# Kernel tuning notes

Hardware: AMD Instinct MI355X
Metric: run time of the kernel (lower is better)

The kernel has to match this reference:

```python
import jax, jax.numpy as jnp
import numpy as np

N, F = 8000, 256
NEG_SLOPE = 0.2


def setup_inputs() -> dict:
    key = jax.random.key(0)
    k1, k2, k3, k4, k5, k6, k7 = jax.random.split(key, 7)
    node_embeddings = jax.random.normal(k1, (N, F), dtype=jnp.float32)
    adj_matrix = jax.random.randint(k2, (N, N), 0, 2, dtype=jnp.int32)
    # Learned params: W (Linear F->F with bias), a (Linear 2F->1 with bias).
    # a's weight [1, 2F] is split into a_src (first F, applied to H_i) and
    # a_dst (last F, applied to H_j) -- mathematically identical to the
    # concat-then-linear formulation, without the N*N*2F intermediate.
    s = 1.0 / np.sqrt(F)
    W_w = jax.random.uniform(k3, (F, F), dtype=jnp.float32, minval=-s, maxval=s)
    W_b = jax.random.uniform(k4, (F,), dtype=jnp.float32, minval=-s, maxval=s)
    s2 = 1.0 / np.sqrt(2 * F)
    a_src = jax.random.uniform(k5, (F,), dtype=jnp.float32, minval=-s2, maxval=s2)
    a_dst = jax.random.uniform(k6, (F,), dtype=jnp.float32, minval=-s2, maxval=s2)
    a_b = jax.random.uniform(k7, (), dtype=jnp.float32, minval=-s2, maxval=s2)
    return {
        "node_embeddings": node_embeddings,
        "adj_matrix": adj_matrix,
        "W_w": W_w,
        "W_b": W_b,
        "a_src": a_src,
        "a_dst": a_dst,
        "a_b": a_b,
    }


def reference(node_embeddings, adj_matrix, W_w, W_b, a_src, a_dst, a_b):
    # H = W(x)
    H = node_embeddings @ W_w.T + W_b                      # [N, F]
    # e_ij = a([H_i ; H_j]) = H_i . a_src + H_j . a_dst + b
    e = (H @ a_src)[:, None] + (H @ a_dst)[None, :] + a_b  # [N, N]
    # mask BEFORE leakyrelu (as in the original), then leakyrelu, then softmax
    e = jnp.where(adj_matrix == 0, -jnp.inf, e)
    e = jnp.where(e >= 0, e, NEG_SLOPE * e)                # leakyrelu(-inf) = -inf
    attn = jax.nn.softmax(e, axis=1)                       # [N, N]
    return attn @ H                                        # [N, F]
```

## Files before the change

### kernel.cpp

```cpp
#include <hip/hip_runtime.h>

#define NN 8000
#define FD 256
#define NEG_SLOPE 0.2f
#define BI 64
#define KT 64
#define JS 4

typedef __bf16 bf16;
typedef __bf16 bf16x8 __attribute__((ext_vector_type(8)));
typedef float f32x4 __attribute__((ext_vector_type(4)));

__global__ __launch_bounds__(256) void k_linear(const float* __restrict__ X,
                                                const float* __restrict__ W,
                                                const float* __restrict__ b,
                                                bf16* __restrict__ Ht,
                                                float* __restrict__ outT,
                                                float* __restrict__ lg) {
    __shared__ float Xs[16][260];
    const int t = threadIdx.x;
    const int i0 = blockIdx.x * 16;
    {
        const int gt = blockIdx.x * 256 + t;
        const float4 z4 = {0.f, 0.f, 0.f, 0.f};
        float4* o4 = (float4*)outT;
        #pragma unroll
        for (int k = 0; k < 4; ++k) o4[gt + k * 128000] = z4;
        if (gt < NN) lg[gt] = 0.f;
    }
    #pragma unroll
    for (int r = 0; r < 16; ++r)
        Xs[r][t] = X[(size_t)(i0 + r) * FD + t];
    __syncthreads();
    const int f = t;
    float acc[16];
    const float bf_ = b[f];
    #pragma unroll
    for (int ii = 0; ii < 16; ++ii) acc[ii] = bf_;
    for (int k4 = 0; k4 < FD / 4; ++k4) {
        const float4 w4 = *(const float4*)&W[(size_t)f * FD + k4 * 4];
        #pragma unroll
        for (int ii = 0; ii < 16; ++ii) {
            const float4 x4 = *(const float4*)&Xs[ii][k4 * 4];
            acc[ii] += x4.x * w4.x + x4.y * w4.y + x4.z * w4.z + x4.w * w4.w;
        }
    }
    bf16x8 v0, v1;
    #pragma unroll
    for (int ii = 0; ii < 8; ++ii) { v0[ii] = (bf16)acc[ii]; v1[ii] = (bf16)acc[ii + 8]; }
    *(bf16x8*)&Ht[(size_t)f * NN + i0]     = v0;
    *(bf16x8*)&Ht[(size_t)f * NN + i0 + 8] = v1;
}

__global__ __launch_bounds__(256) void k_attn_vec(const bf16* __restrict__ Ht,
                                                  const float* __restrict__ a_src,
                                                  const float* __restrict__ a_dst,
                                                  const float* __restrict__ a_b,
                                                  float* __restrict__ hs,
                                                  float* __restrict__ hd) {
    __shared__ float psh[4][64], pdh[4][64];
    const int t = threadIdx.x;
    const int li = t & 63;
    const int q = t >> 6;
    const int i = blockIdx.x * 64 + li;
    float ps = 0.f, pd = 0.f;
    #pragma unroll 8
    for (int fi = 0; fi < 64; ++fi) {
        const int f = q * 64 + fi;
        const float h = (float)Ht[(size_t)f * NN + i];
        ps += h * a_src[f];
        pd += h * a_dst[f];
    }
    psh[q][li] = ps; pdh[q][li] = pd;
    __syncthreads();
    if (q == 0) {
        ps = psh[0][li] + psh[1][li] + psh[2][li] + psh[3][li];
        pd = pdh[0][li] + pdh[1][li] + pdh[2][li] + pdh[3][li];
        hs[i] = ps + a_b[0];
        hd[i] = pd;
    }
}

__device__ __forceinline__ bf16x8 wgen(int4 alo, int4 ahi, float4 hlo, float4 hhi,
                                       float hsv, float& ls) {
    float w[8]; float e;
    e = hsv + hlo.x; e = e >= 0.f ? e : NEG_SLOPE * e; w[0] = alo.x ? __expf(e) : 0.f;
    e = hsv + hlo.y; e = e >= 0.f ? e : NEG_SLOPE * e; w[1] = alo.y ? __expf(e) : 0.f;
    e = hsv + hlo.z; e = e >= 0.f ? e : NEG_SLOPE * e; w[2] = alo.z ? __expf(e) : 0.f;
    e = hsv + hlo.w; e = e >= 0.f ? e : NEG_SLOPE * e; w[3] = alo.w ? __expf(e) : 0.f;
    e = hsv + hhi.x; e = e >= 0.f ? e : NEG_SLOPE * e; w[4] = ahi.x ? __expf(e) : 0.f;
    e = hsv + hhi.y; e = e >= 0.f ? e : NEG_SLOPE * e; w[5] = ahi.y ? __expf(e) : 0.f;
    e = hsv + hhi.z; e = e >= 0.f ? e : NEG_SLOPE * e; w[6] = ahi.z ? __expf(e) : 0.f;
    e = hsv + hhi.w; e = e >= 0.f ? e : NEG_SLOPE * e; w[7] = ahi.w ? __expf(e) : 0.f;
    ls += ((w[0] + w[1]) + (w[2] + w[3])) + ((w[4] + w[5]) + (w[6] + w[7]));
    bf16x8 r;
    #pragma unroll
    for (int i = 0; i < 8; ++i) r[i] = (bf16)w[i];
    return r;
}

__global__ __launch_bounds__(256, 2) void k_gat(const bf16* __restrict__ Ht,
                                                const int* __restrict__ adj,
                                                const float* __restrict__ hs,
                                                const float* __restrict__ hd,
                                                float* __restrict__ outT,
                                                float* __restrict__ lg) {
    __shared__ __attribute__((aligned(16))) bf16 As[2][FD * KT];

    const int t  = threadIdx.x;
    const int l  = t & 63;
    const int wv = t >> 6;
    const int ib = blockIdx.x >> 2;
    const int jb = blockIdx.x & 3;
    const int i0 = ib * BI;
    const int jq0 = jb * 2048;
    const int NS = (jb < 3) ? 32 : 29;

    const int al = l & 15, asl = l >> 4;
    const int i = i0 + wv * 16 + al;
    const float hsv = hs[i];
    const int*   adjp = adj + (size_t)i * NN + jq0 + asl * 8;
    const float* hdp  = hd + jq0 + asl * 8;

    auto stage = [&](int s_, int bufi) {
        #pragma unroll
        for (int q = 0; q < 8; ++q) {
            const int idx = q * 256 + t;
            const int row = idx >> 3;
            const int sslot = (idx & 7) ^ (row & 7);
            const bf16* src = Ht + (size_t)row * NN + jq0 + s_ * KT + sslot * 8;
            bf16* dst = &As[bufi][idx * 8];
            __builtin_amdgcn_global_load_lds(
                (const __attribute__((address_space(1))) void*)src,
                (__attribute__((address_space(3))) void*)dst, 16, 0, 0);
        }
    };

    stage(0, 0);
    int4 aj0 = *(const int4*)adjp,        aj1 = *(const int4*)(adjp + 4);
    int4 aj2 = *(const int4*)(adjp + 32), aj3 = *(const int4*)(adjp + 36);
    float4 hc0 = *(const float4*)hdp,        hc1 = *(const float4*)(hdp + 4);
    float4 hc2 = *(const float4*)(hdp + 32), hc3 = *(const float4*)(hdp + 36);

    f32x4 acc[16];
    #pragma unroll
    for (int ff = 0; ff < 16; ++ff) acc[ff] = (f32x4){0.f, 0.f, 0.f, 0.f};
    float lsum = 0.f;

    #pragma unroll 1
    for (int s = 0; s < NS; ++s) {
        const int cur = s & 1;
        int4 na0, na1, na2, na3; float4 nh0, nh1, nh2, nh3;
        if (s + 1 < NS) {
            stage(s + 1, cur ^ 1);
            const int o = (s + 1) * KT;
            na0 = *(const int4*)(adjp + o);      na1 = *(const int4*)(adjp + o + 4);
            na2 = *(const int4*)(adjp + o + 32); na3 = *(const int4*)(adjp + o + 36);
            nh0 = *(const float4*)(hdp + o);      nh1 = *(const float4*)(hdp + o + 4);
            nh2 = *(const float4*)(hdp + o + 32); nh3 = *(const float4*)(hdp + o + 36);
        }

        const bf16x8 b0 = wgen(aj0, aj1, hc0, hc1, hsv, lsum);
        const bf16x8 b1 = wgen(aj2, aj3, hc2, hc3, hsv, lsum);

        if (s + 1 < NS) asm volatile("s_waitcnt vmcnt(16)" ::: "memory");
        else            asm volatile("s_waitcnt vmcnt(0)" ::: "memory");
        __builtin_amdgcn_s_barrier();

        {
            const char* Ab = (const char*)&As[cur][0];
            #pragma unroll
            for (int ff = 0; ff < 16; ++ff) {
                const int rb = (ff * 16 + al) * 128;
                const bf16x8 a0 = *(const bf16x8*)(Ab + rb + ((asl ^ (al & 7)) << 4));
                const bf16x8 a1 = *(const bf16x8*)(Ab + rb + (((4 + asl) ^ (al & 7)) << 4));
                acc[ff] = __builtin_amdgcn_mfma_f32_16x16x32_bf16(a0, b0, acc[ff], 0, 0, 0);
                acc[ff] = __builtin_amdgcn_mfma_f32_16x16x32_bf16(a1, b1, acc[ff], 0, 0, 0);
            }
        }
        asm volatile("s_waitcnt lgkmcnt(0)" ::: "memory");
        __builtin_amdgcn_s_barrier();

        aj0 = na0; aj1 = na1; aj2 = na2; aj3 = na3;
        hc0 = nh0; hc1 = nh1; hc2 = nh2; hc3 = nh3;
    }

    lsum += __shfl_xor(lsum, 16);
    lsum += __shfl_xor(lsum, 32);
    if (asl == 0) atomicAdd(&lg[i], lsum);

    #pragma unroll
    for (int ff = 0; ff < 16; ++ff) {
        #pragma unroll
        for (int g = 0; g < 4; ++g) {
            atomicAdd(&outT[(size_t)(ff * 16 + asl * 4 + g) * NN + i], acc[ff][g]);
        }
    }
}

__global__ __launch_bounds__(256) void k_norm(const float* __restrict__ outT,
                                              const float* __restrict__ lg,
                                              float* __restrict__ out) {
    __shared__ float Ts[64][65];
    const int t = threadIdx.x;
    const int tx = t & 63, ty = t >> 6;
    const int ib = blockIdx.x >> 2, fb = blockIdx.x & 3;
    const int i0 = ib * 64, f0 = fb * 64;
    #pragma unroll
    for (int r = 0; r < 16; ++r) {
        const int f = ty * 16 + r;
        Ts[f][tx] = outT[(size_t)(f0 + f) * NN + i0 + tx];
    }
    __syncthreads();
    #pragma unroll
    for (int r = 0; r < 16; ++r) {
        const int irow = ty * 16 + r;
        const float rinv = 1.0f / lg[i0 + irow];
        out[(size_t)(i0 + irow) * FD + f0 + tx] = Ts[tx][irow] * rinv;
    }
}

extern "C" void kernel_launch(void* const* d_in, const int* in_sizes, int n_in,
                              void* d_out, int out_size, void* d_ws, size_t ws_size,
                              hipStream_t stream) {
    const float* X     = (const float*)d_in[0];
    const int*   adj   = (const int*)d_in[1];
    const float* Ww    = (const float*)d_in[2];
    const float* Wb    = (const float*)d_in[3];
    const float* a_src = (const float*)d_in[4];
    const float* a_dst = (const float*)d_in[5];
    const float* a_b   = (const float*)d_in[6];
    float* out = (float*)d_out;

    bf16*  Ht   = (bf16*)d_ws;
    float* hs   = (float*)((char*)d_ws + (size_t)FD * NN * sizeof(bf16));
    float* hd   = hs + NN;
    float* lg   = hd + NN;
    float* outT = lg + NN;

    k_linear<<<NN / 16, 256, 0, stream>>>(X, Ww, Wb, Ht, outT, lg);
    k_attn_vec<<<NN / 64, 256, 0, stream>>>(Ht, a_src, a_dst, a_b, hs, hd);
    k_gat<<<(NN / BI) * JS, 256, 0, stream>>>(Ht, adj, hs, hd, outT, lg);
    k_norm<<<(NN / 64) * (FD / 64), 256, 0, stream>>>(outT, lg, out);
}
```

Before: 155.2 us.

## Split GAT waves into 2x2 feature/row tiles with KT=32 stages

Reorganizes the k_gat wave tiling so each wave computes half the feature dimension for two 16-row groups instead of all 256 features for one 16-row group. Each LDS A-fragment now feeds two MFMAs, and the K tile per stage is halved to 32, which halves the shared buffer and changes the swizzle. The j range per block becomes 2016 with 63/61 stages. This doubles the adj loads per wave, since each wave now reads two rows, and adds twice as many barriers and stage iterations. In exchange it cuts LDS A-reads per MFMA.

```diff
diff --git a/kernel.cpp b/kernel.cpp
--- a/kernel.cpp
+++ b/kernel.cpp
@@ -4,7 +4,7 @@
 #define FD 256
 #define NEG_SLOPE 0.2f
 #define BI 64
-#define KT 64
+#define KT 32
 #define JS 4
 
 typedef __bf16 bf16;
@@ -110,24 +110,29 @@
     const int t  = threadIdx.x;
     const int l  = t & 63;
     const int wv = t >> 6;
+    const int fh = wv & 1;
+    const int ih = wv >> 1;
     const int ib = blockIdx.x >> 2;
     const int jb = blockIdx.x & 3;
     const int i0 = ib * BI;
-    const int jq0 = jb * 2048;
-    const int NS = (jb < 3) ? 32 : 29;
+    const int jq0 = jb * 2016;
+    const int NS = (jb < 3) ? 63 : 61;
 
     const int al = l & 15, asl = l >> 4;
-    const int i = i0 + wv * 16 + al;
-    const float hsv = hs[i];
-    const int*   adjp = adj + (size_t)i * NN + jq0 + asl * 8;
-    const float* hdp  = hd + jq0 + asl * 8;
+    const int ia = i0 + ih * 32 + al;
+    const int ibx = ia + 16;
+    const float hsv0 = hs[ia];
+    const float hsv1 = hs[ibx];
+    const int* adjp0 = adj + (size_t)ia  * NN + jq0 + asl * 8;
+    const int* adjp1 = adj + (size_t)ibx * NN + jq0 + asl * 8;
+    const float* hdp = hd + jq0 + asl * 8;
 
     auto stage = [&](int s_, int bufi) {
         #pragma unroll
-        for (int q = 0; q < 8; ++q) {
+        for (int q = 0; q < 4; ++q) {
             const int idx = q * 256 + t;
-            const int row = idx >> 3;
-            const int sslot = (idx & 7) ^ (row & 7);
+            const int row = idx >> 2;
+            const int sslot = (idx & 3) ^ ((row >> 1) & 3);
             const bf16* src = Ht + (size_t)row * NN + jq0 + s_ * KT + sslot * 8;
             bf16* dst = &As[bufi][idx * 8];
             __builtin_amdgcn_global_load_lds(
@@ -136,64 +141,69 @@
         }
     };
 
+    int4 a00 = *(const int4*)adjp0, a01 = *(const int4*)(adjp0 + 4);
+    int4 a10 = *(const int4*)adjp1, a11 = *(const int4*)(adjp1 + 4);
+    float4 h0 = *(const float4*)hdp, h1 = *(const float4*)(hdp + 4);
     stage(0, 0);
-    int4 aj0 = *(const int4*)adjp,        aj1 = *(const int4*)(adjp + 4);
-    int4 aj2 = *(const int4*)(adjp + 32), aj3 = *(const int4*)(adjp + 36);
-    float4 hc0 = *(const float4*)hdp,        hc1 = *(const float4*)(hdp + 4);
-    float4 hc2 = *(const float4*)(hdp + 32), hc3 = *(const float4*)(hdp + 36);
-
-    f32x4 acc[16];
-    #pragma unroll
-    for (int ff = 0; ff < 16; ++ff) acc[ff] = (f32x4){0.f, 0.f, 0.f, 0.f};
-    float lsum = 0.f;
+
+    f32x4 acc[8][2];
+    #pragma unroll
+    for (int ff = 0; ff < 8; ++ff) {
+        acc[ff][0] = (f32x4){0.f, 0.f, 0.f, 0.f};
+        acc[ff][1] = (f32x4){0.f, 0.f, 0.f, 0.f};
+    }
+    float ls0 = 0.f, ls1 = 0.f;
 
     #pragma unroll 1
     for (int s = 0; s < NS; ++s) {
         const int cur = s & 1;
-        int4 na0, na1, na2, na3; float4 nh0, nh1, nh2, nh3;
+        int4 na00, na01, na10, na11; float4 nh0, nh1;
         if (s + 1 < NS) {
+            const int o = (s + 1) * KT;
+            na00 = *(const int4*)(adjp0 + o); na01 = *(const int4*)(adjp0 + o + 4);
+            na10 = *(const int4*)(adjp1 + o); na11 = *(const int4*)(adjp1 + o + 4);
+            nh0  = *(const float4*)(hdp + o); nh1  = *(const float4*)(hdp + o + 4);
             stage(s + 1, cur ^ 1);
-            const int o = (s + 1) * KT;
-            na0 = *(const int4*)(adjp + o);      na1 = *(const int4*)(adjp + o + 4);
-            na2 = *(const int4*)(adjp + o + 32); na3 = *(const int4*)(adjp + o + 36);
-            nh0 = *(const float4*)(hdp + o);      nh1 = *(const float4*)(hdp + o + 4);
-            nh2 = *(const float4*)(hdp + o + 32); nh3 = *(const float4*)(hdp + o + 36);
-        }
-
-        const bf16x8 b0 = wgen(aj0, aj1, hc0, hc1, hsv, lsum);
-        const bf16x8 b1 = wgen(aj2, aj3, hc2, hc3, hsv, lsum);
-
-        if (s + 1 < NS) asm volatile("s_waitcnt vmcnt(16)" ::: "memory");
+        }
+
+        const bf16x8 b0 = wgen(a00, a01, h0, h1, hsv0, ls0);
+        const bf16x8 b1 = wgen(a10, a11, h0, h1, hsv1, ls1);
+
+        if (s + 1 < NS) asm volatile("s_waitcnt vmcnt(10)" ::: "memory");
         else            asm volatile("s_waitcnt vmcnt(0)" ::: "memory");
         __builtin_amdgcn_s_barrier();
 
         {
             const char* Ab = (const char*)&As[cur][0];
             #pragma unroll
-            for (int ff = 0; ff < 16; ++ff) {
-                const int rb = (ff * 16 + al) * 128;
-                const bf16x8 a0 = *(const bf16x8*)(Ab + rb + ((asl ^ (al & 7)) << 4));
-                const bf16x8 a1 = *(const bf16x8*)(Ab + rb + (((4 + asl) ^ (al & 7)) << 4));
-                acc[ff] = __builtin_amdgcn_mfma_f32_16x16x32_bf16(a0, b0, acc[ff], 0, 0, 0);
-                acc[ff] = __builtin_amdgcn_mfma_f32_16x16x32_bf16(a1, b1, acc[ff], 0, 0, 0);
+            for (int ff = 0; ff < 8; ++ff) {
+                const int row = fh * 128 + ff * 16 + al;
+                const bf16x8 a = *(const bf16x8*)(Ab + row * 64 +
+                                                  ((asl ^ ((row >> 1) & 3)) << 4));
+                acc[ff][0] = __builtin_amdgcn_mfma_f32_16x16x32_bf16(a, b0, acc[ff][0], 0, 0, 0);
+                acc[ff][1] = __builtin_amdgcn_mfma_f32_16x16x32_bf16(a, b1, acc[ff][1], 0, 0, 0);
             }
         }
         asm volatile("s_waitcnt lgkmcnt(0)" ::: "memory");
         __builtin_amdgcn_s_barrier();
 
-        aj0 = na0; aj1 = na1; aj2 = na2; aj3 = na3;
-        hc0 = nh0; hc1 = nh1; hc2 = nh2; hc3 = nh3;
-    }
-
-    lsum += __shfl_xor(lsum, 16);
-    lsum += __shfl_xor(lsum, 32);
-    if (asl == 0) atomicAdd(&lg[i], lsum);
-
-    #pragma unroll
-    for (int ff = 0; ff < 16; ++ff) {
+        a00 = na00; a01 = na01; a10 = na10; a11 = na11; h0 = nh0; h1 = nh1;
+    }
+
+    ls0 += __shfl_xor(ls0, 16); ls0 += __shfl_xor(ls0, 32);
+    ls1 += __shfl_xor(ls1, 16); ls1 += __shfl_xor(ls1, 32);
+    if (fh == 0 && asl == 0) {
+        atomicAdd(&lg[ia],  ls0);
+        atomicAdd(&lg[ibx], ls1);
+    }
+
+    #pragma unroll
+    for (int ff = 0; ff < 8; ++ff) {
         #pragma unroll
         for (int g = 0; g < 4; ++g) {
-            atomicAdd(&outT[(size_t)(ff * 16 + asl * 4 + g) * NN + i], acc[ff][g]);
+            const int f = fh * 128 + ff * 16 + asl * 4 + g;
+            atomicAdd(&outT[(size_t)f * NN + ia],  acc[ff][0][g]);
+            atomicAdd(&outT[(size_t)f * NN + ibx], acc[ff][1][g]);
         }
     }
 }
```

Measured after the change: 193.8 us. +24.9%, slower.
